# Optimization experiments

Measured on AMD Instinct MI355X. Metric: run time of the kernel, lower is better.

The kernel has to match this reference:

```python
import jax, jax.numpy as jnp
import numpy as np

D = 300      # GloVe embed size (hard-coded in module)
H = 150      # per-direction LSTM hidden (bi-output = 300 = hidden_size)
EPS = 1e-8   # torch F.cosine_similarity eps


def setup_inputs() -> dict:
    key = jax.random.key(0)
    ks = jax.random.split(key, 16)
    B, S, C, T = 256, 128, 256, 64
    n = lambda k, sh, sc=1.0: jax.random.normal(k, sh, dtype=jnp.float32) * sc
    return {
        "src_emb": n(ks[0], (B, S, D)),
        "col_emb": n(ks[1], (B, C, D)),
        "tab_emb": n(ks[2], (B, T, D)),
        "col_hot": (jax.random.uniform(ks[3], (B, C, 9)) < 0.3).astype(jnp.float32),
        "tab_hot": (jax.random.uniform(ks[4], (B, T, 5)) < 0.3).astype(jnp.float32),
        # BiLSTM params (gate order i,f,g,o)
        "Wx_f": n(ks[5], (D, 4 * H), 0.05), "Wh_f": n(ks[6], (H, 4 * H), 0.05), "b_f": jnp.zeros((4 * H,), jnp.float32),
        "Wx_b": n(ks[7], (D, 4 * H), 0.05), "Wh_b": n(ks[8], (H, 4 * H), 0.05), "b_b": jnp.zeros((4 * H,), jnp.float32),
        # type encoders (Linear 9->300, 5->300)
        "W_col": n(ks[9], (9, 2 * H), 0.1), "b_col": jnp.zeros((2 * H,), jnp.float32),
        "W_tab": n(ks[10], (5, 2 * H), 0.1), "b_tab": jnp.zeros((2 * H,), jnp.float32),
    }


def _lstm_dir(x_tbd, Wx, Wh, b, reverse):
    # x_tbd: [T, B, D] -> hs: [T, B, H], cT: [B, H]
    Bsz = x_tbd.shape[1]
    h0 = jnp.zeros((Bsz, H), x_tbd.dtype)
    def step(carry, xt):
        h, c = carry
        g = xt @ Wx + h @ Wh + b
        i, f, gg, o = jnp.split(g, 4, axis=-1)
        c = jax.nn.sigmoid(f) * c + jax.nn.sigmoid(i) * jnp.tanh(gg)
        h = jax.nn.sigmoid(o) * jnp.tanh(c)
        return (h, c), h
    (hT, cT), hs = jax.lax.scan(step, (h0, h0), x_tbd, reverse=reverse)
    return hs, cT


def _embed_context(src_enc, src_emb, cmp_emb):
    # cosine sim [B,C,S] then weighted sum of src_enc -> [B,C,2H]
    sn = jnp.maximum(jnp.linalg.norm(src_emb, axis=-1), EPS)   # [B,S]
    cn = jnp.maximum(jnp.linalg.norm(cmp_emb, axis=-1), EPS)   # [B,C]
    sim = jnp.einsum("bcd,bsd->bcs", cmp_emb, src_emb) / (cn[:, :, None] * sn[:, None, :])
    return jnp.einsum("bcs,bsd->bcd", sim, src_enc)


def reference(src_emb, col_emb, tab_emb, col_hot, tab_hot,
              Wx_f, Wh_f, b_f, Wx_b, Wh_b, b_b,
              W_col, b_col, W_tab, b_tab):
    x = jnp.transpose(src_emb, (1, 0, 2))               # [S,B,D]
    hs_f, c_f = _lstm_dir(x, Wx_f, Wh_f, b_f, False)
    hs_b, c_b = _lstm_dir(x, Wx_b, Wh_b, b_b, True)
    src_encoding = jnp.transpose(jnp.concatenate([hs_f, hs_b], -1), (1, 0, 2))  # [B,S,300]
    last_cell = jnp.concatenate([c_f, c_b], -1)          # [B,300]
    # dropout is identity in eval mode
    col_encoding = col_emb + _embed_context(src_encoding, src_emb, col_emb) + (col_hot @ W_col + b_col)
    tab_encoding = tab_emb + _embed_context(src_encoding, src_emb, tab_emb) + (tab_hot @ W_tab + b_tab)
    return src_encoding, col_encoding, tab_encoding, last_cell
```

## Files before the change

### kernel.cpp

```cpp
#include <hip/hip_runtime.h>
#include <math.h>

#define Bv 256
#define Sv 128
#define Cv 256
#define Tv 64
#define Dv 300
#define Hv 150
#define G4v 600

typedef _Float16 h8v __attribute__((ext_vector_type(8)));
typedef _Float16 h4v __attribute__((ext_vector_type(4)));
typedef float    f4v __attribute__((ext_vector_type(4)));
typedef float    f2v __attribute__((ext_vector_type(2)));

__global__ __launch_bounds__(256)
void row_norm_k(const float* __restrict__ x, int rows, float* __restrict__ out)
{
    int gtid = blockIdx.x * 256 + threadIdx.x;
    int wave = gtid >> 6;
    int lane = threadIdx.x & 63;
    if (wave >= rows) return;
    const float* row = x + (size_t)wave * Dv;
    float s = 0.f;
    for (int k = lane; k < Dv; k += 64) { float v = row[k]; s += v * v; }
    #pragma unroll
    for (int off = 32; off > 0; off >>= 1) s += __shfl_down(s, off, 64);
    if (lane == 0) out[wave] = fmaxf(sqrtf(s), 1e-8f);
}

__global__ __launch_bounds__(256)
void conv_a16_k(const float* __restrict__ A, _Float16* __restrict__ A16)
{
    int idx = blockIdx.x * 256 + threadIdx.x;
    int row = idx / 80;
    int k   = (idx - row * 80) * 4;
    float4 v = {0.f, 0.f, 0.f, 0.f};
    if (k < Dv) v = *(const float4*)&A[(size_t)row * Dv + k];
    h4v o;
    o[0] = (_Float16)v.x; o[1] = (_Float16)v.y;
    o[2] = (_Float16)v.z; o[3] = (_Float16)v.w;
    *(h4v*)&A16[(size_t)row * 320 + k] = o;
}

__global__ __launch_bounds__(320)
void conv_w16_k(const float* __restrict__ Wf, const float* __restrict__ Wb,
                _Float16* __restrict__ W16T)
{
    const int n   = blockIdx.x;
    const int dir = blockIdx.y;
    const int k   = threadIdx.x;
    const float* W = dir ? Wb : Wf;
    float v = (k < Dv && n < G4v) ? W[(size_t)k * G4v + n] : 0.f;
    W16T[((size_t)dir * 640 + n) * 320 + k] = (_Float16)v;
}

__global__ __launch_bounds__(256)
void gemm_xw_mfma_k(const _Float16* __restrict__ A16,
                    const _Float16* __restrict__ W16T,
                    const float* __restrict__ bf, const float* __restrict__ bb,
                    _Float16* __restrict__ Gout)
{
    const int m0  = blockIdx.x * 128;
    const int n0  = blockIdx.y * 128;
    const int dir = blockIdx.z;
    const float* bias = dir ? bb : bf;
    const _Float16* Wd = W16T + (size_t)dir * 640 * 320;

    __shared__ _Float16 As[128][40];
    __shared__ _Float16 Bs[128][40];

    const int tid  = threadIdx.x;
    const int lane = tid & 63;
    const int w    = tid >> 6;
    const int wm   = w >> 1, wn = w & 1;
    const int r16  = lane & 15, q = lane >> 4;

    const int srow  = tid >> 1;
    const int sslot = (tid & 1) * 16;

    f4v acc[4][4];
    #pragma unroll
    for (int i = 0; i < 4; ++i)
        #pragma unroll
        for (int j = 0; j < 4; ++j) acc[i][j] = (f4v){0.f,0.f,0.f,0.f};

    for (int k0 = 0; k0 < 320; k0 += 32) {
        h8v av0 = *(const h8v*)&A16[(size_t)(m0 + srow) * 320 + k0 + sslot];
        h8v av1 = *(const h8v*)&A16[(size_t)(m0 + srow) * 320 + k0 + sslot + 8];
        h8v bv0 = *(const h8v*)&Wd [(size_t)(n0 + srow) * 320 + k0 + sslot];
        h8v bv1 = *(const h8v*)&Wd [(size_t)(n0 + srow) * 320 + k0 + sslot + 8];
        __syncthreads();
        *(h8v*)&As[srow][sslot]     = av0;
        *(h8v*)&As[srow][sslot + 8] = av1;
        *(h8v*)&Bs[srow][sslot]     = bv0;
        *(h8v*)&Bs[srow][sslot + 8] = bv1;
        __syncthreads();

        h8v af[4], bfr[4];
        #pragma unroll
        for (int mi = 0; mi < 4; ++mi)
            af[mi] = *(const h8v*)&As[wm*64 + mi*16 + r16][q*8];
        #pragma unroll
        for (int ni = 0; ni < 4; ++ni)
            bfr[ni] = *(const h8v*)&Bs[wn*64 + ni*16 + r16][q*8];
        #pragma unroll
        for (int mi = 0; mi < 4; ++mi)
            #pragma unroll
            for (int ni = 0; ni < 4; ++ni)
                acc[mi][ni] = __builtin_amdgcn_mfma_f32_16x16x32_f16(
                                  af[mi], bfr[ni], acc[mi][ni], 0, 0, 0);
    }

    #pragma unroll
    for (int ni = 0; ni < 4; ++ni) {
        int n = n0 + wn*64 + ni*16 + r16;
        if (n >= G4v) continue;
        float bn = bias[n];
        #pragma unroll
        for (int mi = 0; mi < 4; ++mi) {
            #pragma unroll
            for (int r = 0; r < 4; ++r) {
                int row = m0 + wm*64 + mi*16 + q*4 + r;
                int b   = row >> 7;
                int s   = row & 127;
                Gout[(((size_t)dir * Sv + s) * Bv + b) * G4v + n] =
                    (_Float16)(acc[mi][ni][r] + bn);
            }
        }
    }
}

__device__ __forceinline__ float sigm_f(float x)
{
    return __builtin_amdgcn_rcpf(1.f + __expf(-x));
}
__device__ __forceinline__ float tanh_f(float x)
{
    float e = __expf(-2.f * __builtin_fabsf(x));
    float r = (1.f - e) * __builtin_amdgcn_rcpf(1.f + e);
    return __builtin_copysignf(r, x);
}

__global__ __launch_bounds__(640, 1)
void lstm_mfma_k(const _Float16* __restrict__ G16,
                 const float* __restrict__ Wh_f, const float* __restrict__ Wh_b,
                 float* __restrict__ out_src,
                 float* __restrict__ out_cell)
{
    const int blk = blockIdx.x;
    const int dir = blk & 1;
    const int b0  = (blk >> 1) * 4;
    const float* Wh = dir ? Wh_b : Wh_f;
    const _Float16* Gd = G16 + (size_t)dir * Sv * Bv * G4v;

    const int tid  = threadIdx.x;
    const int w    = tid >> 6;
    const int lane = tid & 63;
    const int q    = lane >> 4;
    const int cp   = lane & 15;
    const int hcol = w * 16 + cp;
    const bool colok = (hcol < Hv);
    const int hc   = colok ? hcol : 0;
    const int rp   = q;

    __shared__ _Float16 h_sh[2][16][168];
    __shared__ float    g_sh[10][4][16][4];

    h8v Bf[4][5];
    #pragma unroll
    for (int g = 0; g < 4; ++g) {
        #pragma unroll
        for (int ks = 0; ks < 5; ++ks) {
            h8v v;
            #pragma unroll
            for (int j = 0; j < 8; ++j) {
                int k = 32*ks + 8*q + j;
                float x = (k < Hv && colok) ? Wh[(size_t)k * G4v + g*Hv + hcol] : 0.f;
                v[j] = (_Float16)x;
            }
            Bf[g][ks] = v;
        }
    }

    for (int i = tid; i < 2*16*168; i += 640)
        ((_Float16*)h_sh)[i] = (_Float16)0.f;

    float c = 0.f;

    _Float16 gA[4], gB[4];
    {
        int ss0 = dir ? (Sv - 1) : 0;
        int ss1 = dir ? (Sv - 2) : 1;
        const _Float16* p0 = Gd + ((size_t)ss0 * Bv + b0 + rp) * G4v;
        const _Float16* p1 = Gd + ((size_t)ss1 * Bv + b0 + rp) * G4v;
        #pragma unroll
        for (int g = 0; g < 4; ++g) {
            gA[g] = p0[g*Hv + hc];
            gB[g] = p1[g*Hv + hc];
        }
    }
    __syncthreads();

    int cur = 0;
    for (int s = 0; s < Sv; ++s) {
        const int ss = dir ? (Sv - 1 - s) : s;

        _Float16 gC[4];
        #pragma unroll
        for (int g = 0; g < 4; ++g) gC[g] = (_Float16)0.f;
        if (s + 2 < Sv) {
            int ss2 = dir ? (ss - 2) : (ss + 2);
            const _Float16* p = Gd + ((size_t)ss2 * Bv + b0 + rp) * G4v;
            #pragma unroll
            for (int g = 0; g < 4; ++g) gC[g] = p[g*Hv + hc];
        }

        f4v a0 = {0.f,0.f,0.f,0.f}, a1 = a0, a2 = a0, a3 = a0;
        #pragma unroll
        for (int ks = 0; ks < 5; ++ks) {
            h8v af = *(const h8v*)&h_sh[cur][cp][32*ks + 8*q];
            a0 = __builtin_amdgcn_mfma_f32_16x16x32_f16(af, Bf[0][ks], a0, 0, 0, 0);
            a1 = __builtin_amdgcn_mfma_f32_16x16x32_f16(af, Bf[1][ks], a1, 0, 0, 0);
            a2 = __builtin_amdgcn_mfma_f32_16x16x32_f16(af, Bf[2][ks], a2, 0, 0, 0);
            a3 = __builtin_amdgcn_mfma_f32_16x16x32_f16(af, Bf[3][ks], a3, 0, 0, 0);
        }

        if (q == 0) {
            *(f4v*)&g_sh[w][0][cp][0] = a0;
            *(f4v*)&g_sh[w][1][cp][0] = a1;
            *(f4v*)&g_sh[w][2][cp][0] = a2;
            *(f4v*)&g_sh[w][3][cp][0] = a3;
        }
        float gi = g_sh[w][0][cp][rp] + (float)gA[0];
        float gf = g_sh[w][1][cp][rp] + (float)gA[1];
        float gg = g_sh[w][2][cp][rp] + (float)gA[2];
        float go = g_sh[w][3][cp][rp] + (float)gA[3];

        float I  = sigm_f(gi);
        float F  = sigm_f(gf);
        float Gt = tanh_f(gg);
        float O  = sigm_f(go);
        c = F * c + I * Gt;
        float h = O * tanh_f(c);

        h_sh[cur ^ 1][rp][hcol] = (_Float16)h;
        if (colok)
            out_src[(((size_t)(b0 + rp)) * Sv + ss) * (2*Hv) + dir*Hv + hcol] = h;

        #pragma unroll
        for (int g = 0; g < 4; ++g) { gA[g] = gB[g]; gB[g] = gC[g]; }
        cur ^= 1;

        asm volatile("s_waitcnt lgkmcnt(0)" ::: "memory");
        __builtin_amdgcn_s_barrier();
        __builtin_amdgcn_sched_barrier(0);
    }

    if (colok)
        out_cell[(size_t)(b0 + rp) * (2*Hv) + dir*Hv + hcol] = c;
}

__global__ __launch_bounds__(256)
void trans_enc_k(const float* __restrict__ enc,
                 _Float16* __restrict__ hi, _Float16* __restrict__ lo)
{
    const int b  = blockIdx.z;
    const int s0 = blockIdx.x * 64;
    const int n0 = blockIdx.y * 64;
    __shared__ float t[64][65];
    const int tid = threadIdx.x;
    const int j  = tid & 63;
    const int i0 = (tid >> 6) * 16;
    #pragma unroll
    for (int ii = 0; ii < 16; ++ii) {
        int i = i0 + ii;
        int n = n0 + j;
        t[i][j] = (n < Dv) ? enc[((size_t)b*Sv + s0 + i)*Dv + n] : 0.f;
    }
    __syncthreads();
    #pragma unroll
    for (int ii = 0; ii < 16; ++ii) {
        int nr = i0 + ii;
        float v = t[j][nr];
        _Float16 hh = (_Float16)v;
        float l = v - (float)hh;
        size_t o = ((size_t)b*320 + n0 + nr)*128 + s0 + j;
        hi[o] = hh;
        lo[o] = (_Float16)l;
    }
}

__global__ __launch_bounds__(256)
void gemm_sim_mfma_k(const _Float16* __restrict__ cmp16,
                     const _Float16* __restrict__ src16,
                     const float* __restrict__ cn, const float* __restrict__ sn,
                     int M, _Float16* __restrict__ sim16)
{
    const int m0 = blockIdx.x * 128;
    const int b  = blockIdx.z;
    const _Float16* A  = cmp16 + (size_t)b * M * 320;
    const _Float16* Bm = src16 + (size_t)b * 128 * 320;

    __shared__ _Float16 As[128][40];
    __shared__ _Float16 Bs[128][40];

    const int tid  = threadIdx.x;
    const int lane = tid & 63;
    const int w    = tid >> 6;
    const int wm   = w >> 1, wn = w & 1;
    const int r16  = lane & 15, q = lane >> 4;

    const int srow  = tid >> 1;
    const int sslot = (tid & 1) * 16;
    const int arow  = (m0 + srow < M) ? (m0 + srow) : 0;

    f4v acc[4][4];
    #pragma unroll
    for (int i = 0; i < 4; ++i)
        #pragma unroll
        for (int j = 0; j < 4; ++j) acc[i][j] = (f4v){0.f,0.f,0.f,0.f};

    for (int k0 = 0; k0 < 320; k0 += 32) {
        h8v av0 = *(const h8v*)&A [(size_t)arow * 320 + k0 + sslot];
        h8v av1 = *(const h8v*)&A [(size_t)arow * 320 + k0 + sslot + 8];
        h8v bv0 = *(const h8v*)&Bm[(size_t)srow * 320 + k0 + sslot];
        h8v bv1 = *(const h8v*)&Bm[(size_t)srow * 320 + k0 + sslot + 8];
        __syncthreads();
        *(h8v*)&As[srow][sslot]     = av0;
        *(h8v*)&As[srow][sslot + 8] = av1;
        *(h8v*)&Bs[srow][sslot]     = bv0;
        *(h8v*)&Bs[srow][sslot + 8] = bv1;
        __syncthreads();

        h8v af[4], bfr[4];
        #pragma unroll
        for (int mi = 0; mi < 4; ++mi)
            af[mi] = *(const h8v*)&As[wm*64 + mi*16 + r16][q*8];
        #pragma unroll
        for (int ni = 0; ni < 4; ++ni)
            bfr[ni] = *(const h8v*)&Bs[wn*64 + ni*16 + r16][q*8];
        #pragma unroll
        for (int mi = 0; mi < 4; ++mi)
            #pragma unroll
            for (int ni = 0; ni < 4; ++ni)
                acc[mi][ni] = __builtin_amdgcn_mfma_f32_16x16x32_f16(
                                  af[mi], bfr[ni], acc[mi][ni], 0, 0, 0);
    }

    #pragma unroll
    for (int ni = 0; ni < 4; ++ni) {
        int s = wn*64 + ni*16 + r16;
        float snv = sn[(size_t)b * 128 + s];
        #pragma unroll
        for (int mi = 0; mi < 4; ++mi) {
            #pragma unroll
            for (int r = 0; r < 4; ++r) {
                int m = m0 + wm*64 + mi*16 + q*4 + r;
                if (m < M) {
                    float v = acc[mi][ni][r] / (cn[(size_t)b * M + m] * snv);
                    sim16[((size_t)b * M + m) * 128 + s] = (_Float16)v;
                }
            }
        }
    }
}

__global__ __launch_bounds__(256, 2)
void gemm_ctx_fused_k(const _Float16* __restrict__ sim16,
                      const _Float16* __restrict__ encHi,
                      const _Float16* __restrict__ encLo,
                      const float* __restrict__ emb,
                      const float* __restrict__ hot,
                      const float* __restrict__ W,
                      const float* __restrict__ bias,
                      int M, int hd, float* __restrict__ outp)
{
    const int b  = blockIdx.z;
    const int m0 = blockIdx.x * 64;
    const int tid = threadIdx.x;
    const int lane = tid & 63;
    const int w = tid >> 6;
    const int q = lane >> 4, cp = lane & 15;

    __shared__ _Float16 As[64][136];
    __shared__ float Wsh[9*304];
    __shared__ float bsh[304];
    __shared__ float hotsh[64*9];

    {
        const int srow = tid >> 2;
        const int scol = (tid & 3) * 32;
        const _Float16* src = sim16 + ((size_t)b * M + m0 + srow) * 128 + scol;
        *(h8v*)&As[srow][scol]      = *(const h8v*)&src[0];
        *(h8v*)&As[srow][scol + 8]  = *(const h8v*)&src[8];
        *(h8v*)&As[srow][scol + 16] = *(const h8v*)&src[16];
        *(h8v*)&As[srow][scol + 24] = *(const h8v*)&src[24];
    }
    for (int i = tid; i < hd*304; i += 256) {
        int jj = i / 304, nn = i - jj*304;
        Wsh[i] = (nn < Dv) ? W[(size_t)jj * Dv + nn] : 0.f;
    }
    for (int i = tid; i < 304; i += 256) bsh[i] = (i < Dv) ? bias[i] : 0.f;
    for (int i = tid; i < 64*hd; i += 256) hotsh[i] = hot[((size_t)b * M + m0) * hd + i];
    __syncthreads();

    h8v af[4][4];
    #pragma unroll
    for (int mi = 0; mi < 4; ++mi)
        #pragma unroll
        for (int ks = 0; ks < 4; ++ks)
            af[mi][ks] = *(const h8v*)&As[mi*16 + cp][32*ks + 8*q];

    f4v acc[4][5];
    #pragma unroll
    for (int mi = 0; mi < 4; ++mi)
        #pragma unroll
        for (int nt = 0; nt < 5; ++nt) acc[mi][nt] = (f4v){0.f,0.f,0.f,0.f};

    const int nbase = w * 80;
    #pragma unroll
    for (int pass = 0; pass < 2; ++pass) {
        const _Float16* encp = pass ? encLo : encHi;
        #pragma unroll
        for (int nt = 0; nt < 5; ++nt) {
            int n = nbase + nt*16 + cp;
            const _Float16* bp = encp + ((size_t)b * 320 + n) * 128 + 8*q;
            h8v b0 = *(const h8v*)&bp[0];
            h8v b1 = *(const h8v*)&bp[32];
            h8v b2 = *(const h8v*)&bp[64];
            h8v b3 = *(const h8v*)&bp[96];
            #pragma unroll
            for (int mi = 0; mi < 4; ++mi) {
                acc[mi][nt] = __builtin_amdgcn_mfma_f32_16x16x32_f16(af[mi][0], b0, acc[mi][nt], 0, 0, 0);
                acc[mi][nt] = __builtin_amdgcn_mfma_f32_16x16x32_f16(af[mi][1], b1, acc[mi][nt], 0, 0, 0);
                acc[mi][nt] = __builtin_amdgcn_mfma_f32_16x16x32_f16(af[mi][2], b2, acc[mi][nt], 0, 0, 0);
                acc[mi][nt] = __builtin_amdgcn_mfma_f32_16x16x32_f16(af[mi][3], b3, acc[mi][nt], 0, 0, 0);
            }
        }
    }

    #pragma unroll
    for (int nt = 0; nt < 5; ++nt) {
        int n = nbase + nt*16 + cp;
        if (n >= Dv) continue;
        float bn = bsh[n];
        #pragma unroll
        for (int mi = 0; mi < 4; ++mi) {
            #pragma unroll
            for (int r = 0; r < 4; ++r) {
                int ml = mi*16 + 4*q + r;
                int m  = m0 + ml;
                float v = acc[mi][nt][r] + bn + emb[((size_t)b * M + m) * Dv + n];
                for (int jj = 0; jj < hd; ++jj)
                    v = fmaf(hotsh[ml*hd + jj], Wsh[jj*304 + n], v);
                outp[((size_t)b * M + m) * Dv + n] = v;
            }
        }
    }
}

extern "C" void kernel_launch(void* const* d_in, const int* in_sizes, int n_in,
                              void* d_out, int out_size, void* d_ws, size_t ws_size,
                              hipStream_t stream)
{
    (void)in_sizes; (void)n_in; (void)out_size; (void)ws_size;
    const float* src_emb = (const float*)d_in[0];
    const float* col_emb = (const float*)d_in[1];
    const float* tab_emb = (const float*)d_in[2];
    const float* col_hot = (const float*)d_in[3];
    const float* tab_hot = (const float*)d_in[4];
    const float* Wx_f = (const float*)d_in[5];
    const float* Wh_f = (const float*)d_in[6];
    const float* b_f  = (const float*)d_in[7];
    const float* Wx_b = (const float*)d_in[8];
    const float* Wh_b = (const float*)d_in[9];
    const float* b_b  = (const float*)d_in[10];
    const float* W_col = (const float*)d_in[11];
    const float* b_col = (const float*)d_in[12];
    const float* W_tab = (const float*)d_in[13];
    const float* b_tab = (const float*)d_in[14];

    float* out      = (float*)d_out;
    float* out_src  = out;
    float* out_col  = out + 9830400;
    float* out_tab  = out + 29491200;
    float* out_cell = out + 34406400;

    float* ws = (float*)d_ws;
    _Float16* Gbuf16 = (_Float16*)ws;
    _Float16* encHi    = (_Float16*)(ws);
    _Float16* encLo    = (_Float16*)(ws + 5242880);
    _Float16* sim16_col= (_Float16*)(ws + 11000000);
    _Float16* sim16_tab= (_Float16*)(ws + 16000000);
    float* sn = ws + 39321600;
    float* cn = sn + 32768;
    float* tn = cn + 65536;

    _Float16* A16   = (_Float16*)(out + 9830400);
    _Float16* W16T  = A16 + (size_t)32768 * 320;
    _Float16* col16 = (_Float16*)(out + 15278080);
    _Float16* tab16 = (_Float16*)(out + 29491200);

    conv_a16_k<<<32768*80/256, 256, 0, stream>>>(src_emb, A16);
    conv_a16_k<<<65536*80/256, 256, 0, stream>>>(col_emb, col16);
    conv_a16_k<<<16384*80/256, 256, 0, stream>>>(tab_emb, tab16);
    conv_w16_k<<<dim3(640, 2), 320, 0, stream>>>(Wx_f, Wx_b, W16T);

    row_norm_k<<<32768/4, 256, 0, stream>>>(src_emb, 32768, sn);
    row_norm_k<<<65536/4, 256, 0, stream>>>(col_emb, 65536, cn);
    row_norm_k<<<16384/4, 256, 0, stream>>>(tab_emb, 16384, tn);

    gemm_xw_mfma_k<<<dim3(256, 5, 2), 256, 0, stream>>>(A16, W16T, b_f, b_b, Gbuf16);

    lstm_mfma_k<<<128, 640, 0, stream>>>(Gbuf16, Wh_f, Wh_b, out_src, out_cell);

    trans_enc_k<<<dim3(2, 5, 256), 256, 0, stream>>>(out_src, encHi, encLo);

    gemm_sim_mfma_k<<<dim3(2, 1, 256), 256, 0, stream>>>(col16, A16, cn, sn, 256, sim16_col);
    gemm_sim_mfma_k<<<dim3(1, 1, 256), 256, 0, stream>>>(tab16, A16, tn, sn, 64,  sim16_tab);

    gemm_ctx_fused_k<<<dim3(4, 1, 256), 256, 0, stream>>>(
        sim16_col, encHi, encLo, col_emb, col_hot, W_col, b_col, 256, 9, out_col);
    gemm_ctx_fused_k<<<dim3(1, 1, 256), 256, 0, stream>>>(
        sim16_tab, encHi, encLo, tab_emb, tab_hot, W_tab, b_tab, 64, 5, out_tab);
}
```

Measured before the change: 623.8 us.

## Fuse fp16 conversion with row norms and split LSTM to one batch per block

The separate fp16-conversion and row-norm kernels are merged into one pass that reads each embedding row once, writes the fp16 copy and computes its norm. The LSTM kernel now handles one batch row per block instead of four, launching 512 blocks instead of 128 and allowing up to five blocks per CU. This spreads the latency-bound recurrence across more CUs. In exchange three quarters of each block's MFMA rows and gate loads do no useful work.

```diff
diff --git a/kernel.cpp b/kernel.cpp
--- a/kernel.cpp
+++ b/kernel.cpp
@@ -15,32 +15,30 @@
 typedef float    f2v __attribute__((ext_vector_type(2)));
 
 __global__ __launch_bounds__(256)
-void row_norm_k(const float* __restrict__ x, int rows, float* __restrict__ out)
+void fused_cn_k(const float* __restrict__ A, int rows,
+                _Float16* __restrict__ A16, float* __restrict__ nrm)
 {
     int gtid = blockIdx.x * 256 + threadIdx.x;
-    int wave = gtid >> 6;
+    int row  = gtid >> 6;
     int lane = threadIdx.x & 63;
-    if (wave >= rows) return;
-    const float* row = x + (size_t)wave * Dv;
+    if (row >= rows) return;
+    const float* rp = A   + (size_t)row * Dv;
+    _Float16*    op = A16 + (size_t)row * 320;
     float s = 0.f;
-    for (int k = lane; k < Dv; k += 64) { float v = row[k]; s += v * v; }
+    #pragma unroll
+    for (int i4 = lane; i4 < 80; i4 += 64) {
+        int k = i4 * 4;
+        float4 v = {0.f, 0.f, 0.f, 0.f};
+        if (k < Dv) v = *(const float4*)&rp[k];
+        h4v o;
+        o[0] = (_Float16)v.x; o[1] = (_Float16)v.y;
+        o[2] = (_Float16)v.z; o[3] = (_Float16)v.w;
+        *(h4v*)&op[k] = o;
+        s += v.x*v.x + v.y*v.y + v.z*v.z + v.w*v.w;
+    }
     #pragma unroll
     for (int off = 32; off > 0; off >>= 1) s += __shfl_down(s, off, 64);
-    if (lane == 0) out[wave] = fmaxf(sqrtf(s), 1e-8f);
-}
-
-__global__ __launch_bounds__(256)
-void conv_a16_k(const float* __restrict__ A, _Float16* __restrict__ A16)
-{
-    int idx = blockIdx.x * 256 + threadIdx.x;
-    int row = idx / 80;
-    int k   = (idx - row * 80) * 4;
-    float4 v = {0.f, 0.f, 0.f, 0.f};
-    if (k < Dv) v = *(const float4*)&A[(size_t)row * Dv + k];
-    h4v o;
-    o[0] = (_Float16)v.x; o[1] = (_Float16)v.y;
-    o[2] = (_Float16)v.z; o[3] = (_Float16)v.w;
-    *(h4v*)&A16[(size_t)row * 320 + k] = o;
+    if (lane == 0) nrm[row] = fmaxf(sqrtf(s), 1e-8f);
 }
 
 __global__ __launch_bounds__(320)
@@ -142,7 +140,7 @@
     return __builtin_copysignf(r, x);
 }
 
-__global__ __launch_bounds__(640, 1)
+__global__ __launch_bounds__(640, 5)
 void lstm_mfma_k(const _Float16* __restrict__ G16,
                  const float* __restrict__ Wh_f, const float* __restrict__ Wh_b,
                  float* __restrict__ out_src,
@@ -150,7 +148,7 @@
 {
     const int blk = blockIdx.x;
     const int dir = blk & 1;
-    const int b0  = (blk >> 1) * 4;
+    const int b   = blk >> 1;
     const float* Wh = dir ? Wh_b : Wh_f;
     const _Float16* Gd = G16 + (size_t)dir * Sv * Bv * G4v;
 
@@ -163,6 +161,7 @@
     const bool colok = (hcol < Hv);
     const int hc   = colok ? hcol : 0;
     const int rp   = q;
+    const bool bok = (rp == 0);
 
     __shared__ _Float16 h_sh[2][16][168];
     __shared__ float    g_sh[10][4][16][4];
@@ -189,11 +188,13 @@
     float c = 0.f;
 
     _Float16 gA[4], gB[4];
-    {
+    #pragma unroll
+    for (int g = 0; g < 4; ++g) { gA[g] = (_Float16)0.f; gB[g] = (_Float16)0.f; }
+    if (bok) {
         int ss0 = dir ? (Sv - 1) : 0;
         int ss1 = dir ? (Sv - 2) : 1;
-        const _Float16* p0 = Gd + ((size_t)ss0 * Bv + b0 + rp) * G4v;
-        const _Float16* p1 = Gd + ((size_t)ss1 * Bv + b0 + rp) * G4v;
+        const _Float16* p0 = Gd + ((size_t)ss0 * Bv + b) * G4v;
+        const _Float16* p1 = Gd + ((size_t)ss1 * Bv + b) * G4v;
         #pragma unroll
         for (int g = 0; g < 4; ++g) {
             gA[g] = p0[g*Hv + hc];
@@ -209,9 +210,9 @@
         _Float16 gC[4];
         #pragma unroll
         for (int g = 0; g < 4; ++g) gC[g] = (_Float16)0.f;
-        if (s + 2 < Sv) {
+        if (bok && s + 2 < Sv) {
             int ss2 = dir ? (ss - 2) : (ss + 2);
-            const _Float16* p = Gd + ((size_t)ss2 * Bv + b0 + rp) * G4v;
+            const _Float16* p = Gd + ((size_t)ss2 * Bv + b) * G4v;
             #pragma unroll
             for (int g = 0; g < 4; ++g) gC[g] = p[g*Hv + hc];
         }
@@ -245,8 +246,8 @@
         float h = O * tanh_f(c);
 
         h_sh[cur ^ 1][rp][hcol] = (_Float16)h;
-        if (colok)
-            out_src[(((size_t)(b0 + rp)) * Sv + ss) * (2*Hv) + dir*Hv + hcol] = h;
+        if (bok && colok)
+            out_src[((size_t)b * Sv + ss) * (2*Hv) + dir*Hv + hcol] = h;
 
         #pragma unroll
         for (int g = 0; g < 4; ++g) { gA[g] = gB[g]; gB[g] = gC[g]; }
@@ -257,8 +258,8 @@
         __builtin_amdgcn_sched_barrier(0);
     }
 
-    if (colok)
-        out_cell[(size_t)(b0 + rp) * (2*Hv) + dir*Hv + hcol] = c;
+    if (bok && colok)
+        out_cell[(size_t)b * (2*Hv) + dir*Hv + hcol] = c;
 }
 
 __global__ __launch_bounds__(256)
@@ -502,18 +503,14 @@
     _Float16* col16 = (_Float16*)(out + 15278080);
     _Float16* tab16 = (_Float16*)(out + 29491200);
 
-    conv_a16_k<<<32768*80/256, 256, 0, stream>>>(src_emb, A16);
-    conv_a16_k<<<65536*80/256, 256, 0, stream>>>(col_emb, col16);
-    conv_a16_k<<<16384*80/256, 256, 0, stream>>>(tab_emb, tab16);
+    fused_cn_k<<<32768/4, 256, 0, stream>>>(src_emb, 32768, A16,   sn);
+    fused_cn_k<<<65536/4, 256, 0, stream>>>(col_emb, 65536, col16, cn);
+    fused_cn_k<<<16384/4, 256, 0, stream>>>(tab_emb, 16384, tab16, tn);
     conv_w16_k<<<dim3(640, 2), 320, 0, stream>>>(Wx_f, Wx_b, W16T);
 
-    row_norm_k<<<32768/4, 256, 0, stream>>>(src_emb, 32768, sn);
-    row_norm_k<<<65536/4, 256, 0, stream>>>(col_emb, 65536, cn);
-    row_norm_k<<<16384/4, 256, 0, stream>>>(tab_emb, 16384, tn);
-
     gemm_xw_mfma_k<<<dim3(256, 5, 2), 256, 0, stream>>>(A16, W16T, b_f, b_b, Gbuf16);
 
-    lstm_mfma_k<<<128, 640, 0, stream>>>(Gbuf16, Wh_f, Wh_b, out_src, out_cell);
+    lstm_mfma_k<<<512, 640, 0, stream>>>(Gbuf16, Wh_f, Wh_b, out_src, out_cell);
 
     trans_enc_k<<<dim3(2, 5, 256), 256, 0, stream>>>(out_src, encHi, encLo);
 
```

Result: slower. 1.270 ms (+103.5%).
